# Optimization experiments

Measured on AMD Instinct MI355X. Metric: run time of the kernel, lower is better.

The kernel has to match this reference:

```python
import jax, jax.numpy as jnp
import numpy as np

B, S, HID = 8, 4096, 4096
NH, HD, ROT = 32, 128, 64  # heads, head_dim, rotary_dim (rotary_percentage=0.5)
FFN = 16384
EPS = 1e-5
SCALE = HD ** -0.5


def _ln1p(x, w, b):
    # LayerNorm1P: layer_norm with (weight + 1)
    mu = jnp.mean(x, axis=-1, keepdims=True)
    var = jnp.var(x, axis=-1, keepdims=True)
    return (x - mu) * jax.lax.rsqrt(var + EPS) * (w + 1.0) + b


def _rope(x, pos):
    # x: [B, NH, ROT] (rotary slice), pos: [B] int. GPT-NeoX style (rotate halves).
    half = ROT // 2
    inv_freq = 1.0 / (10000.0 ** (jnp.arange(0, ROT, 2, dtype=jnp.float32) / ROT))
    ang = pos[:, None].astype(jnp.float32) * inv_freq       # [B, half]
    cos = jnp.cos(ang)[:, None, :].astype(x.dtype)           # [B, 1, half]
    sin = jnp.sin(ang)[:, None, :].astype(x.dtype)
    x1, x2 = x[..., :half], x[..., half:]
    return jnp.concatenate([x1 * cos - x2 * sin, x2 * cos + x1 * sin], axis=-1)


def setup_inputs() -> dict:
    key = jax.random.key(0)
    ks = jax.random.split(key, 12)
    w = lambda k, shp: (jax.random.normal(k, shp, jnp.float32) * 0.02)
    return {
        "hidden_states": jax.random.normal(ks[0], (B, HID), jnp.float32),
        "k_cache": jax.random.normal(ks[1], (B, S, NH, HD), jnp.float32),
        "v_cache": jax.random.normal(ks[2], (B, S, NH, HD), jnp.float32),
        "w_qkv": w(ks[3], (HID, 3 * HID)),
        "w_dense": w(ks[4], (HID, HID)),
        "w_fc1": w(ks[5], (HID, 2 * FFN)),
        "w_fc2": w(ks[6], (FFN, HID)),
        "ln1_w": jax.random.normal(ks[7], (HID,), jnp.float32) * 0.02,
        "ln1_b": jnp.zeros((HID,), jnp.float32),
        "ln2_w": jax.random.normal(ks[8], (HID,), jnp.float32) * 0.02,
        "ln2_b": jnp.zeros((HID,), jnp.float32),
        "positions": jax.random.randint(ks[9], (B,), 0, S, jnp.int64),
    }


def reference(hidden_states, k_cache, v_cache, w_qkv, w_dense, w_fc1, w_fc2,
              ln1_w, ln1_b, ln2_w, ln2_b, positions):
    residual = hidden_states
    x = _ln1p(hidden_states, ln1_w, ln1_b)

    # fused QKV projection, chunk along last dim
    qkv = x @ w_qkv                                          # [B, 3*HID]
    q, k, v = jnp.split(qkv, 3, axis=-1)
    q = q.reshape(B, NH, HD)
    k = k.reshape(B, NH, HD)
    v = v.reshape(B, NH, HD)

    # inline RoPE on first ROT dims of q and new k
    q = jnp.concatenate([_rope(q[..., :ROT], positions), q[..., ROT:]], axis=-1)
    k = jnp.concatenate([_rope(k[..., :ROT], positions), k[..., ROT:]], axis=-1)

    # write new token's k/v into the paged KV cache at its slot
    bidx = jnp.arange(B)
    k_cache = k_cache.at[bidx, positions].set(k)
    v_cache = v_cache.at[bidx, positions].set(v)

    # single-query paged attention over cached keys, causal to current position
    scores = jnp.einsum('bhd,bshd->bhs', q, k_cache) * SCALE  # [B, NH, S]
    valid = jnp.arange(S)[None, None, :] <= positions[:, None, None]
    scores = jnp.where(valid, scores, jnp.finfo(scores.dtype).min)
    probs = jax.nn.softmax(scores, axis=-1)
    attn = jnp.einsum('bhs,bshd->bhd', probs, v_cache).reshape(B, HID)

    hidden_states = residual + attn @ w_dense

    residual = hidden_states
    x = _ln1p(hidden_states, ln2_w, ln2_b)
    h = x @ w_fc1                                            # [B, 2*FFN]
    h1, h2 = jnp.split(h, 2, axis=-1)
    x = (jax.nn.silu(h1) * h2) @ w_fc2                       # SwiGLU
    return residual + x
```

## Files before the change

### kernel.cpp

```cpp
#include <hip/hip_runtime.h>
#include <cstddef>
#include <cstdint>

#define NB 8
#define SEQ 4096
#define HIDDIM 4096
#define NHEAD 32
#define HDIM 128
#define FFNDIM 16384
#define ATTN_SCALE 0.08838834764831845f

__device__ __forceinline__ float wave_sum(float v) {
#pragma unroll
  for (int off = 32; off > 0; off >>= 1) v += __shfl_xor(v, off, 64);
  return v;
}

__device__ __forceinline__ int get_pos(const int* __restrict__ p, int b) {
  const bool is64 = ((p[1] | p[3] | p[5] | p[7]) == 0);
  return is64 ? p[2 * b] : p[b];
}

__global__ __launch_bounds__(256) void ln_rows(const float* __restrict__ in,
                                               const float* __restrict__ w,
                                               const float* __restrict__ bias,
                                               float* __restrict__ out_t) {
  __shared__ float row[HIDDIM];
  __shared__ float red[4];
  const int b = blockIdx.x, t = threadIdx.x;
  float s = 0.f;
  for (int i = t; i < HIDDIM; i += 256) {
    const float v = in[(size_t)b * HIDDIM + i];
    row[i] = v;
    s += v;
  }
  s = wave_sum(s);
  if ((t & 63) == 0) red[t >> 6] = s;
  __syncthreads();
  const float mean = (red[0] + red[1] + red[2] + red[3]) * (1.0f / HIDDIM);
  __syncthreads();
  float vs = 0.f;
  for (int i = t; i < HIDDIM; i += 256) {
    const float d = row[i] - mean;
    vs += d * d;
  }
  vs = wave_sum(vs);
  if ((t & 63) == 0) red[t >> 6] = vs;
  __syncthreads();
  const float var = (red[0] + red[1] + red[2] + red[3]) * (1.0f / HIDDIM);
  const float rs = rsqrtf(var + 1e-5f);
  for (int i = t; i < HIDDIM; i += 256) {
    out_t[(size_t)i * NB + b] = (row[i] - mean) * rs * (w[i] + 1.0f) + bias[i];
  }
}

template <int KCHUNK>
__global__ __launch_bounds__(256) void gemm8(const float* __restrict__ W,
                                             const float* __restrict__ xt,
                                             float* __restrict__ part, int N) {
  const int j0 = (blockIdx.x * 256 + threadIdx.x) * 4;
  const size_t i0 = (size_t)blockIdx.y * KCHUNK;
  const float* __restrict__ wp = W + i0 * N + j0;
  const float* __restrict__ xp = xt + i0 * NB;
  float4 a0 = {0, 0, 0, 0}, a1 = {0, 0, 0, 0}, a2 = {0, 0, 0, 0}, a3 = {0, 0, 0, 0};
  float4 a4 = {0, 0, 0, 0}, a5 = {0, 0, 0, 0}, a6 = {0, 0, 0, 0}, a7 = {0, 0, 0, 0};
#pragma unroll 4
  for (int i = 0; i < KCHUNK; ++i) {
    const float4 w = *reinterpret_cast<const float4*>(wp + (size_t)i * N);
    const float4 xa = *reinterpret_cast<const float4*>(xp + i * NB);
    const float4 xb = *reinterpret_cast<const float4*>(xp + i * NB + 4);
#define ACC4(A, sxx)                                                          \
  A.x = fmaf(sxx, w.x, A.x);                                                  \
  A.y = fmaf(sxx, w.y, A.y);                                                  \
  A.z = fmaf(sxx, w.z, A.z);                                                  \
  A.w = fmaf(sxx, w.w, A.w);
    ACC4(a0, xa.x) ACC4(a1, xa.y) ACC4(a2, xa.z) ACC4(a3, xa.w)
    ACC4(a4, xb.x) ACC4(a5, xb.y) ACC4(a6, xb.z) ACC4(a7, xb.w)
#undef ACC4
  }
  float* op = part + (size_t)blockIdx.y * NB * N + j0;
  *reinterpret_cast<float4*>(op) = a0; op += N;
  *reinterpret_cast<float4*>(op) = a1; op += N;
  *reinterpret_cast<float4*>(op) = a2; op += N;
  *reinterpret_cast<float4*>(op) = a3; op += N;
  *reinterpret_cast<float4*>(op) = a4; op += N;
  *reinterpret_cast<float4*>(op) = a5; op += N;
  *reinterpret_cast<float4*>(op) = a6; op += N;
  *reinterpret_cast<float4*>(op) = a7;
}

__global__ __launch_bounds__(128) void rope_reduce(const float* __restrict__ part, int nchunk,
                                                   const int* __restrict__ posp,
                                                   float* __restrict__ qo,
                                                   float* __restrict__ ko,
                                                   float* __restrict__ vo) {
  const int blk = blockIdx.x;
  const int b = blk >> 5, h = blk & 31;
  const int t = threadIdx.x;
  const int role = t >> 5;
  const int d4 = (t & 31) * 4;
  const int col = h * HDIM + d4;
  __shared__ float qsh[HDIM], ksh[HDIM];
  float4 acc = {0.f, 0.f, 0.f, 0.f};
  if (role < 3) {
    const size_t off = (size_t)role * HIDDIM + col;
    for (int c = 0; c < nchunk; ++c) {
      const float4 p = *reinterpret_cast<const float4*>(
          part + ((size_t)c * NB + b) * (3 * HIDDIM) + off);
      acc.x += p.x; acc.y += p.y; acc.z += p.z; acc.w += p.w;
    }
    if (role == 0) *reinterpret_cast<float4*>(&qsh[d4]) = acc;
    if (role == 1) *reinterpret_cast<float4*>(&ksh[d4]) = acc;
  }
  __syncthreads();
  if (role < 2) {
    const float* sh = role ? ksh : qsh;
    const float pos = (float)get_pos(posp, b);
    float4 o;
    float* ov = &o.x;
#pragma unroll
    for (int j = 0; j < 4; ++j) {
      const int d = d4 + j;
      if (d < 64) {
        const int f = d & 31;
        const float ang = pos * powf(10000.0f, -(float)f * (1.0f / 32.0f));
        const float cs = cosf(ang), sn = sinf(ang);
        ov[j] = (d < 32) ? sh[d] * cs - sh[d + 32] * sn
                         : sh[d] * cs + sh[d - 32] * sn;
      } else {
        ov[j] = sh[d];
      }
    }
    float* dst = (role ? ko : qo) + (size_t)b * HIDDIM + col;
    *reinterpret_cast<float4*>(dst) = o;
  } else if (role == 2) {
    *reinterpret_cast<float4*>(vo + (size_t)b * HIDDIM + col) = acc;
  }
}

__global__ __launch_bounds__(256) void attn_split(
    const float* __restrict__ kc, const float* __restrict__ vc,
    const float* __restrict__ q, const float* __restrict__ kn,
    const float* __restrict__ vn, const int* __restrict__ posp,
    float* __restrict__ Mp, float* __restrict__ Lp, float* __restrict__ Ap) {
  const int c = blockIdx.x, h = blockIdx.y, b = blockIdx.z;
  const int pos = get_pos(posp, b);
  const int s0 = c * 256;
  if (s0 > pos) return;
  const int s1 = min(s0 + 256, pos + 1);
  const int wid = threadIdx.x >> 6, lane = threadIdx.x & 63;
  const int half = lane >> 5;
  const int d4 = (lane & 31) * 4;
  const float4 qv = *reinterpret_cast<const float4*>(q + (size_t)b * HIDDIM + h * HDIM + d4);
  const float* kb = kc + ((size_t)b * SEQ * NHEAD + h) * HDIM + d4;
  const float* vb = vc + ((size_t)b * SEQ * NHEAD + h) * HDIM + d4;
  const float* knp = kn + (size_t)b * HIDDIM + h * HDIM + d4;
  const float* vnp = vn + (size_t)b * HIDDIM + h * HDIM + d4;
  float m = -1e30f, l = 0.f;
  float4 acc = {0.f, 0.f, 0.f, 0.f};
  for (int sb = s0; sb < s1; sb += 8) {
    const int s = sb + wid * 2 + half;
    const float* kp = (s == pos) ? knp : kb + (size_t)s * (NHEAD * HDIM);
    const float* vp = (s == pos) ? vnp : vb + (size_t)s * (NHEAD * HDIM);
    const float4 kk = *reinterpret_cast<const float4*>(kp);
    const float4 vv = *reinterpret_cast<const float4*>(vp);
    float p = qv.x * kk.x + qv.y * kk.y + qv.z * kk.z + qv.w * kk.w;
#pragma unroll
    for (int off = 16; off > 0; off >>= 1) p += __shfl_xor(p, off, 64);
    p = (s < s1) ? p * ATTN_SCALE : -2e30f;
    const float mn = fmaxf(m, p);
    const float cf = __expf(m - mn);
    const float pw = __expf(p - mn);
    l = l * cf + pw;
    acc.x = acc.x * cf + pw * vv.x;
    acc.y = acc.y * cf + pw * vv.y;
    acc.z = acc.z * cf + pw * vv.z;
    acc.w = acc.w * cf + pw * vv.w;
    m = mn;
  }
  __shared__ float sm[8], sl[8], sa[8][HDIM];
  const int st = wid * 2 + half;
  *reinterpret_cast<float4*>(&sa[st][d4]) = acc;
  if ((lane & 31) == 0) { sm[st] = m; sl[st] = l; }
  __syncthreads();
  if (threadIdx.x < HDIM) {
    const int d = threadIdx.x;
    float M = -1e30f;
#pragma unroll
    for (int w2 = 0; w2 < 8; ++w2) M = fmaxf(M, sm[w2]);
    float L = 0.f, A = 0.f;
#pragma unroll
    for (int w2 = 0; w2 < 8; ++w2) {
      const float e = __expf(sm[w2] - M);
      L += e * sl[w2];
      A += e * sa[w2][d];
    }
    const size_t idx = (size_t)(b * NHEAD + h) * 16 + c;
    if (d == 0) { Mp[idx] = M; Lp[idx] = L; }
    Ap[idx * HDIM + d] = A;
  }
}

__global__ __launch_bounds__(128) void attn_combine(
    const float* __restrict__ Mp, const float* __restrict__ Lp,
    const float* __restrict__ Ap, const int* __restrict__ posp,
    float* __restrict__ out_t) {
  const int blk = blockIdx.x;
  const int b = blk >> 5, h = blk & 31;
  const int d = threadIdx.x;
  const int nc = get_pos(posp, b) / 256 + 1;
  const size_t base = (size_t)(b * NHEAD + h) * 16;
  float M = -1e30f;
  for (int c = 0; c < nc; ++c) M = fmaxf(M, Mp[base + c]);
  float L = 0.f, A = 0.f;
  for (int c = 0; c < nc; ++c) {
    const float e = __expf(Mp[base + c] - M);
    L += e * Lp[base + c];
    A += e * Ap[(base + c) * HDIM + d];
  }
  out_t[(size_t)(h * HDIM + d) * NB + b] = A / L;
}

__global__ __launch_bounds__(128) void reduce_add(const float* __restrict__ part, int nchunk,
                                                  const float* __restrict__ base,
                                                  float* __restrict__ out) {
  const int i4 = blockIdx.x * 128 + threadIdx.x;
  const float4* b4 = reinterpret_cast<const float4*>(base);
  const float4* p4 = reinterpret_cast<const float4*>(part);
  float4 v = b4[i4];
  for (int c = 0; c < nchunk; ++c) {
    const float4 p = p4[(size_t)c * (NB * HIDDIM / 4) + i4];
    v.x += p.x; v.y += p.y; v.z += p.z; v.w += p.w;
  }
  reinterpret_cast<float4*>(out)[i4] = v;
}

__global__ __launch_bounds__(256) void gate_silu(const float* __restrict__ part, int nchunk,
                                                 float* __restrict__ gt) {
  const int j4 = (blockIdx.x * 256 + threadIdx.x) * 4;
  const int b = blockIdx.y;
  float4 h1 = {0.f, 0.f, 0.f, 0.f}, h2 = {0.f, 0.f, 0.f, 0.f};
  for (int c = 0; c < nchunk; ++c) {
    const float* p = part + ((size_t)c * NB + b) * (2 * FFNDIM);
    const float4 a = *reinterpret_cast<const float4*>(p + j4);
    const float4 g = *reinterpret_cast<const float4*>(p + FFNDIM + j4);
    h1.x += a.x; h1.y += a.y; h1.z += a.z; h1.w += a.w;
    h2.x += g.x; h2.y += g.y; h2.z += g.z; h2.w += g.w;
  }
  const float* h1v = &h1.x;
  const float* h2v = &h2.x;
#pragma unroll
  for (int j = 0; j < 4; ++j) {
    const float g = (h1v[j] / (1.f + __expf(-h1v[j]))) * h2v[j];
    gt[(size_t)(j4 + j) * NB + b] = g;
  }
}

extern "C" void kernel_launch(void* const* d_in, const int* in_sizes, int n_in,
                              void* d_out, int out_size, void* d_ws, size_t ws_size,
                              hipStream_t stream) {
  const float* hs = (const float*)d_in[0];
  const float* kc = (const float*)d_in[1];
  const float* vc = (const float*)d_in[2];
  const float* wqkv = (const float*)d_in[3];
  const float* wdense = (const float*)d_in[4];
  const float* wfc1 = (const float*)d_in[5];
  const float* wfc2 = (const float*)d_in[6];
  const float* ln1w = (const float*)d_in[7];
  const float* ln1b = (const float*)d_in[8];
  const float* ln2w = (const float*)d_in[9];
  const float* ln2b = (const float*)d_in[10];
  const int* posp = (const int*)d_in[11];
  float* out = (float*)d_out;

  float* ws = (float*)d_ws;
  float* x1t = ws;
  float* qws = x1t + 32768;
  float* kws = qws + 32768;
  float* vws = kws + 32768;
  float* attnt = vws + 32768;
  float* hidden2 = attnt + 32768;
  float* x2t = hidden2 + 32768;
  float* gt = x2t + 32768;
  float* Mp = gt + 131072;
  float* Lp = Mp + 4096;
  float* Ap = Lp + 4096;
  float* part = Ap + 524288;

  ln_rows<<<8, 256, 0, stream>>>(hs, ln1w, ln1b, x1t);
  gemm8<128><<<dim3(12, 32), 256, 0, stream>>>(wqkv, x1t, part, 3 * HIDDIM);
  rope_reduce<<<256, 128, 0, stream>>>(part, 32, posp, qws, kws, vws);
  attn_split<<<dim3(16, NHEAD, NB), 256, 0, stream>>>(kc, vc, qws, kws, vws, posp, Mp, Lp, Ap);
  attn_combine<<<256, 128, 0, stream>>>(Mp, Lp, Ap, posp, attnt);
  gemm8<128><<<dim3(4, 32), 256, 0, stream>>>(wdense, attnt, part, HIDDIM);
  reduce_add<<<64, 128, 0, stream>>>(part, 32, hs, hidden2);
  ln_rows<<<8, 256, 0, stream>>>(hidden2, ln2w, ln2b, x2t);
  gemm8<256><<<dim3(32, 16), 256, 0, stream>>>(wfc1, x2t, part, 2 * FFNDIM);
  gate_silu<<<dim3(16, NB), 256, 0, stream>>>(part, 16, gt);
  gemm8<256><<<dim3(4, 64), 256, 0, stream>>>(wfc2, gt, part, HIDDIM);
  reduce_add<<<64, 128, 0, stream>>>(part, 64, hidden2, out);
}
```

Measured before the change: 422.8 us.

## Fuse whole decoder layer into one cooperative persistent kernel with grid syncs

Replaces the twelve separate kernel launches with a single cooperative kernel of 256 blocks that runs every stage, separated by grid-wide barriers. LayerNorm is folded into the GEMM input staging, with statistics computed in one pass (sum and sum of squares). Attention work items are handed out through an atomic counter. The GEMM tiling changes to float2 per thread with smaller K-chunks. The goal is to remove launch overhead and intermediate buffers. The cost is that only 256 blocks run, which may under-occupy the GPU for the bandwidth-bound GEMMs, and each stage pays for a grid barrier.

```diff
diff --git a/kernel.cpp b/kernel.cpp
--- a/kernel.cpp
+++ b/kernel.cpp
@@ -1,6 +1,9 @@
 #include <hip/hip_runtime.h>
+#include <hip/hip_cooperative_groups.h>
 #include <cstddef>
 #include <cstdint>
+
+namespace cg = cooperative_groups;
 
 #define NB 8
 #define SEQ 4096
@@ -9,8 +12,10 @@
 #define HDIM 128
 #define FFNDIM 16384
 #define ATTN_SCALE 0.08838834764831845f
-
-__device__ __forceinline__ float wave_sum(float v) {
+#define NBLK 256
+#define NTHR 512
+
+__device__ __forceinline__ float wave_sum64(float v) {
 #pragma unroll
   for (int off = 32; off > 0; off >>= 1) v += __shfl_xor(v, off, 64);
   return v;
@@ -21,238 +26,362 @@
   return is64 ? p[2 * b] : p[b];
 }
 
-__global__ __launch_bounds__(256) void ln_rows(const float* __restrict__ in,
-                                               const float* __restrict__ w,
-                                               const float* __restrict__ bias,
-                                               float* __restrict__ out_t) {
-  __shared__ float row[HIDDIM];
-  __shared__ float red[4];
-  const int b = blockIdx.x, t = threadIdx.x;
-  float s = 0.f;
-  for (int i = t; i < HIDDIM; i += 256) {
-    const float v = in[(size_t)b * HIDDIM + i];
-    row[i] = v;
+__device__ __forceinline__ void ln_stats(const float* __restrict__ in,
+                                         float* mu, float* rsd, int t) {
+  const int wv = t >> 6, lane = t & 63;
+  float s = 0.f, s2 = 0.f;
+  for (int i = lane; i < HIDDIM; i += 64) {
+    const float v = in[(size_t)wv * HIDDIM + i];
     s += v;
-  }
-  s = wave_sum(s);
-  if ((t & 63) == 0) red[t >> 6] = s;
+    s2 += v * v;
+  }
+  s = wave_sum64(s);
+  s2 = wave_sum64(s2);
+  if (lane == 0) {
+    const float m = s * (1.0f / HIDDIM);
+    mu[wv] = m;
+    rsd[wv] = rsqrtf(s2 * (1.0f / HIDDIM) - m * m + 1e-5f);
+  }
+}
+
+__device__ __forceinline__ void gemm_item(const float* __restrict__ W, int N,
+                                          size_t i0, int nrows, int jbase,
+                                          const float* xs,
+                                          float* __restrict__ partOut, int t) {
+  const int j = jbase + t * 2;
+  const float* __restrict__ wp = W + i0 * N + j;
+  float2 acc[8];
+#pragma unroll
+  for (int b = 0; b < 8; ++b) acc[b] = {0.f, 0.f};
+#pragma unroll 8
+  for (int i = 0; i < nrows; ++i) {
+    const float2 w = *reinterpret_cast<const float2*>(wp + (size_t)i * N);
+    const float* xr = xs + i * 8;
+#pragma unroll
+    for (int b = 0; b < 8; ++b) {
+      acc[b].x = fmaf(xr[b], w.x, acc[b].x);
+      acc[b].y = fmaf(xr[b], w.y, acc[b].y);
+    }
+  }
+#pragma unroll
+  for (int b = 0; b < 8; ++b)
+    *reinterpret_cast<float2*>(partOut + (size_t)b * N + j) = acc[b];
+}
+
+__global__ __launch_bounds__(NTHR, 2) void mega(
+    const float* __restrict__ hs, const float* __restrict__ kcache,
+    const float* __restrict__ vcache, const float* __restrict__ wqkv,
+    const float* __restrict__ wdense, const float* __restrict__ wfc1,
+    const float* __restrict__ wfc2, const float* __restrict__ ln1w,
+    const float* __restrict__ ln1b, const float* __restrict__ ln2w,
+    const float* __restrict__ ln2b, const int* __restrict__ posp,
+    float* __restrict__ out, float* __restrict__ ws) {
+  cg::grid_group gg = cg::this_grid();
+  const int blk = blockIdx.x, t = threadIdx.x;
+
+  float* qws = ws;
+  float* kws = qws + 32768;
+  float* vws = kws + 32768;
+  float* attnt = vws + 32768;
+  float* hidden2 = attnt + 32768;
+  float* gt = hidden2 + 32768;
+  float* Mp = gt + 131072;
+  float* Lp = Mp + 4096;
+  float* Ap = Lp + 4096;
+  unsigned int* ctr = reinterpret_cast<unsigned int*>(Ap + 524288);
+  float* part = reinterpret_cast<float*>(ctr + 64);
+
+  __shared__ float xs[512 * 8];
+  __shared__ float mu[8], rsd[8];
+  __shared__ float qp[4][HDIM], kp[4][HDIM], vp[4][HDIM];
+  __shared__ float sa[16][HDIM];
+  __shared__ float sm[16], sl[16];
+  __shared__ int sitem;
+
+  ln_stats(hs, mu, rsd, t);
   __syncthreads();
-  const float mean = (red[0] + red[1] + red[2] + red[3]) * (1.0f / HIDDIM);
+  for (int it = blk; it < 768; it += NBLK) {
+    const int jt = it % 12;
+    const int ck = it / 12;
+    const size_t i0 = (size_t)ck * 64;
+    {
+      const int i = t >> 3, b = t & 7;
+      const int ii = (int)i0 + i;
+      const float v = hs[(size_t)b * HIDDIM + ii];
+      xs[i * 8 + b] = (v - mu[b]) * rsd[b] * (ln1w[ii] + 1.f) + ln1b[ii];
+    }
+    __syncthreads();
+    gemm_item(wqkv, 3 * HIDDIM, i0, 64, jt * 1024, xs,
+              part + (size_t)ck * 8 * (3 * HIDDIM), t);
+    __syncthreads();
+  }
+  __threadfence();
+  gg.sync();
+
+  {
+    const int b = blk >> 5, h = blk & 31;
+    const int d = t & 127, g = t >> 7;
+    float q = 0.f, k = 0.f, v = 0.f;
+    for (int c = g * 16; c < g * 16 + 16; ++c) {
+      const float* p = part + (size_t)(c * 8 + b) * (3 * HIDDIM) + h * HDIM + d;
+      q += p[0];
+      k += p[HIDDIM];
+      v += p[2 * HIDDIM];
+    }
+    qp[g][d] = q;
+    kp[g][d] = k;
+    vp[g][d] = v;
+    if (blk == 0 && t == 0) *ctr = 0u;
+    __syncthreads();
+    if (t < HDIM) {
+      qp[0][t] = qp[0][t] + qp[1][t] + qp[2][t] + qp[3][t];
+      kp[0][t] = kp[0][t] + kp[1][t] + kp[2][t] + kp[3][t];
+      vp[0][t] = vp[0][t] + vp[1][t] + vp[2][t] + vp[3][t];
+    }
+    __syncthreads();
+    if (t < HDIM) {
+      const int pos = get_pos(posp, b);
+      float qv = qp[0][t], kv = kp[0][t];
+      if (t < 64) {
+        const int f = t & 31;
+        const float ang = (float)pos * powf(10000.0f, -(float)f * (1.0f / 32.0f));
+        const float cs = cosf(ang), sn = sinf(ang);
+        if (t < 32) {
+          qv = qp[0][t] * cs - qp[0][t + 32] * sn;
+          kv = kp[0][t] * cs - kp[0][t + 32] * sn;
+        } else {
+          qv = qp[0][t] * cs + qp[0][t - 32] * sn;
+          kv = kp[0][t] * cs + kp[0][t - 32] * sn;
+        }
+      }
+      const size_t o = (size_t)b * HIDDIM + h * HDIM + t;
+      qws[o] = qv;
+      kws[o] = kv;
+      vws[o] = vp[0][t];
+    }
+  }
+  __threadfence();
+  gg.sync();
+
+  while (true) {
+    if (t == 0) sitem = (int)atomicAdd(ctr, 1u);
+    __syncthreads();
+    const int item = sitem;
+    if (item >= 4096) break;
+    const int c = item >> 8;
+    const int pair = item & 255;
+    const int b = pair & 7, h = pair >> 3;
+    const int pos = get_pos(posp, b);
+    const int s0 = c * 256;
+    if (s0 > pos) {
+      __syncthreads();
+      continue;
+    }
+    const int s1 = min(s0 + 256, pos + 1);
+    const int hw = t >> 5, l32 = t & 31, d4 = l32 * 4;
+    const float4 qv = *reinterpret_cast<const float4*>(
+        qws + (size_t)b * HIDDIM + h * HDIM + d4);
+    const float* kb = kcache + ((size_t)b * SEQ * NHEAD + h) * HDIM + d4;
+    const float* vb = vcache + ((size_t)b * SEQ * NHEAD + h) * HDIM + d4;
+    const float* knp = kws + (size_t)b * HIDDIM + h * HDIM + d4;
+    const float* vnp = vws + (size_t)b * HIDDIM + h * HDIM + d4;
+    float m = -1e30f, l = 0.f;
+    float4 acc = {0.f, 0.f, 0.f, 0.f};
+    const int rbase = s0 + hw * 16;
+#pragma unroll 4
+    for (int r = 0; r < 16; ++r) {
+      const int s = rbase + r;
+      const bool valid = (s < s1);
+      const int sc = valid ? s : s0;
+      const float* kp_ = (sc == pos) ? knp : kb + (size_t)sc * (NHEAD * HDIM);
+      const float* vp_ = (sc == pos) ? vnp : vb + (size_t)sc * (NHEAD * HDIM);
+      const float4 kk = *reinterpret_cast<const float4*>(kp_);
+      const float4 vv = *reinterpret_cast<const float4*>(vp_);
+      float p = qv.x * kk.x + qv.y * kk.y + qv.z * kk.z + qv.w * kk.w;
+#pragma unroll
+      for (int off = 16; off > 0; off >>= 1) p += __shfl_xor(p, off, 64);
+      p = valid ? p * ATTN_SCALE : -2e30f;
+      const float mn = fmaxf(m, p);
+      const float cf = __expf(m - mn);
+      const float pw = __expf(p - mn);
+      l = l * cf + pw;
+      acc.x = acc.x * cf + pw * vv.x;
+      acc.y = acc.y * cf + pw * vv.y;
+      acc.z = acc.z * cf + pw * vv.z;
+      acc.w = acc.w * cf + pw * vv.w;
+      m = mn;
+    }
+    *reinterpret_cast<float4*>(&sa[hw][d4]) = acc;
+    if (l32 == 0) {
+      sm[hw] = m;
+      sl[hw] = l;
+    }
+    __syncthreads();
+    if (t < HDIM) {
+      float M = -1e30f;
+#pragma unroll
+      for (int w2 = 0; w2 < 16; ++w2) M = fmaxf(M, sm[w2]);
+      float L = 0.f, A = 0.f;
+#pragma unroll
+      for (int w2 = 0; w2 < 16; ++w2) {
+        const float e = __expf(sm[w2] - M);
+        L += e * sl[w2];
+        A += e * sa[w2][t];
+      }
+      const size_t idx = (size_t)pair * 16 + c;
+      if (t == 0) {
+        Mp[idx] = M;
+        Lp[idx] = L;
+      }
+      Ap[idx * HDIM + t] = A;
+    }
+    __syncthreads();
+  }
+  __threadfence();
+  gg.sync();
+
+  if (t < HDIM) {
+    const int b = blk & 7, h = blk >> 3;
+    const int pos = get_pos(posp, b);
+    const int nc = pos / 256 + 1;
+    const size_t base = (size_t)blk * 16;
+    float M = -1e30f;
+    for (int c = 0; c < nc; ++c) M = fmaxf(M, Mp[base + c]);
+    float L = 0.f, A = 0.f;
+    for (int c = 0; c < nc; ++c) {
+      const float e = __expf(Mp[base + c] - M);
+      L += e * Lp[base + c];
+      A += e * Ap[(base + c) * HDIM + t];
+    }
+    attnt[(size_t)(h * HDIM + t) * NB + b] = A / L;
+  }
+  __threadfence();
+  gg.sync();
+
+  {
+    const int jt = blk & 3;
+    const int ck = blk >> 2;
+    const size_t i0 = (size_t)ck * 64;
+    xs[t] = attnt[i0 * 8 + t];
+    __syncthreads();
+    gemm_item(wdense, HIDDIM, i0, 64, jt * 1024, xs,
+              part + (size_t)ck * 8 * HIDDIM, t);
+  }
+  __threadfence();
+  gg.sync();
+
+  {
+    const int idx = blk * NTHR + t;
+    const int g = idx >> 2, sub = idx & 3;
+    if (g < 8192) {
+      const float4* p4 = reinterpret_cast<const float4*>(part);
+      float4 v = {0.f, 0.f, 0.f, 0.f};
+      for (int c = sub * 16; c < sub * 16 + 16; ++c) {
+        const float4 p = p4[(size_t)c * 8192 + g];
+        v.x += p.x; v.y += p.y; v.z += p.z; v.w += p.w;
+      }
+#pragma unroll
+      for (int off = 1; off < 4; off <<= 1) {
+        v.x += __shfl_xor(v.x, off, 64);
+        v.y += __shfl_xor(v.y, off, 64);
+        v.z += __shfl_xor(v.z, off, 64);
+        v.w += __shfl_xor(v.w, off, 64);
+      }
+      if (sub == 0) {
+        const float4 hv = reinterpret_cast<const float4*>(hs)[g];
+        float4 o = {v.x + hv.x, v.y + hv.y, v.z + hv.z, v.w + hv.w};
+        reinterpret_cast<float4*>(hidden2)[g] = o;
+      }
+    }
+  }
+  __threadfence();
+  gg.sync();
+
+  ln_stats(hidden2, mu, rsd, t);
   __syncthreads();
-  float vs = 0.f;
-  for (int i = t; i < HIDDIM; i += 256) {
-    const float d = row[i] - mean;
-    vs += d * d;
-  }
-  vs = wave_sum(vs);
-  if ((t & 63) == 0) red[t >> 6] = vs;
-  __syncthreads();
-  const float var = (red[0] + red[1] + red[2] + red[3]) * (1.0f / HIDDIM);
-  const float rs = rsqrtf(var + 1e-5f);
-  for (int i = t; i < HIDDIM; i += 256) {
-    out_t[(size_t)i * NB + b] = (row[i] - mean) * rs * (w[i] + 1.0f) + bias[i];
-  }
-}
-
-template <int KCHUNK>
-__global__ __launch_bounds__(256) void gemm8(const float* __restrict__ W,
-                                             const float* __restrict__ xt,
-                                             float* __restrict__ part, int N) {
-  const int j0 = (blockIdx.x * 256 + threadIdx.x) * 4;
-  const size_t i0 = (size_t)blockIdx.y * KCHUNK;
-  const float* __restrict__ wp = W + i0 * N + j0;
-  const float* __restrict__ xp = xt + i0 * NB;
-  float4 a0 = {0, 0, 0, 0}, a1 = {0, 0, 0, 0}, a2 = {0, 0, 0, 0}, a3 = {0, 0, 0, 0};
-  float4 a4 = {0, 0, 0, 0}, a5 = {0, 0, 0, 0}, a6 = {0, 0, 0, 0}, a7 = {0, 0, 0, 0};
-#pragma unroll 4
-  for (int i = 0; i < KCHUNK; ++i) {
-    const float4 w = *reinterpret_cast<const float4*>(wp + (size_t)i * N);
-    const float4 xa = *reinterpret_cast<const float4*>(xp + i * NB);
-    const float4 xb = *reinterpret_cast<const float4*>(xp + i * NB + 4);
-#define ACC4(A, sxx)                                                          \
-  A.x = fmaf(sxx, w.x, A.x);                                                  \
-  A.y = fmaf(sxx, w.y, A.y);                                                  \
-  A.z = fmaf(sxx, w.z, A.z);                                                  \
-  A.w = fmaf(sxx, w.w, A.w);
-    ACC4(a0, xa.x) ACC4(a1, xa.y) ACC4(a2, xa.z) ACC4(a3, xa.w)
-    ACC4(a4, xb.x) ACC4(a5, xb.y) ACC4(a6, xb.z) ACC4(a7, xb.w)
-#undef ACC4
-  }
-  float* op = part + (size_t)blockIdx.y * NB * N + j0;
-  *reinterpret_cast<float4*>(op) = a0; op += N;
-  *reinterpret_cast<float4*>(op) = a1; op += N;
-  *reinterpret_cast<float4*>(op) = a2; op += N;
-  *reinterpret_cast<float4*>(op) = a3; op += N;
-  *reinterpret_cast<float4*>(op) = a4; op += N;
-  *reinterpret_cast<float4*>(op) = a5; op += N;
-  *reinterpret_cast<float4*>(op) = a6; op += N;
-  *reinterpret_cast<float4*>(op) = a7;
-}
-
-__global__ __launch_bounds__(128) void rope_reduce(const float* __restrict__ part, int nchunk,
-                                                   const int* __restrict__ posp,
-                                                   float* __restrict__ qo,
-                                                   float* __restrict__ ko,
-                                                   float* __restrict__ vo) {
-  const int blk = blockIdx.x;
-  const int b = blk >> 5, h = blk & 31;
-  const int t = threadIdx.x;
-  const int role = t >> 5;
-  const int d4 = (t & 31) * 4;
-  const int col = h * HDIM + d4;
-  __shared__ float qsh[HDIM], ksh[HDIM];
-  float4 acc = {0.f, 0.f, 0.f, 0.f};
-  if (role < 3) {
-    const size_t off = (size_t)role * HIDDIM + col;
-    for (int c = 0; c < nchunk; ++c) {
-      const float4 p = *reinterpret_cast<const float4*>(
-          part + ((size_t)c * NB + b) * (3 * HIDDIM) + off);
-      acc.x += p.x; acc.y += p.y; acc.z += p.z; acc.w += p.w;
-    }
-    if (role == 0) *reinterpret_cast<float4*>(&qsh[d4]) = acc;
-    if (role == 1) *reinterpret_cast<float4*>(&ksh[d4]) = acc;
-  }
-  __syncthreads();
-  if (role < 2) {
-    const float* sh = role ? ksh : qsh;
-    const float pos = (float)get_pos(posp, b);
-    float4 o;
-    float* ov = &o.x;
-#pragma unroll
-    for (int j = 0; j < 4; ++j) {
-      const int d = d4 + j;
-      if (d < 64) {
-        const int f = d & 31;
-        const float ang = pos * powf(10000.0f, -(float)f * (1.0f / 32.0f));
-        const float cs = cosf(ang), sn = sinf(ang);
-        ov[j] = (d < 32) ? sh[d] * cs - sh[d + 32] * sn
-                         : sh[d] * cs + sh[d - 32] * sn;
-      } else {
-        ov[j] = sh[d];
-      }
-    }
-    float* dst = (role ? ko : qo) + (size_t)b * HIDDIM + col;
-    *reinterpret_cast<float4*>(dst) = o;
-  } else if (role == 2) {
-    *reinterpret_cast<float4*>(vo + (size_t)b * HIDDIM + col) = acc;
-  }
-}
-
-__global__ __launch_bounds__(256) void attn_split(
-    const float* __restrict__ kc, const float* __restrict__ vc,
-    const float* __restrict__ q, const float* __restrict__ kn,
-    const float* __restrict__ vn, const int* __restrict__ posp,
-    float* __restrict__ Mp, float* __restrict__ Lp, float* __restrict__ Ap) {
-  const int c = blockIdx.x, h = blockIdx.y, b = blockIdx.z;
-  const int pos = get_pos(posp, b);
-  const int s0 = c * 256;
-  if (s0 > pos) return;
-  const int s1 = min(s0 + 256, pos + 1);
-  const int wid = threadIdx.x >> 6, lane = threadIdx.x & 63;
-  const int half = lane >> 5;
-  const int d4 = (lane & 31) * 4;
-  const float4 qv = *reinterpret_cast<const float4*>(q + (size_t)b * HIDDIM + h * HDIM + d4);
-  const float* kb = kc + ((size_t)b * SEQ * NHEAD + h) * HDIM + d4;
-  const float* vb = vc + ((size_t)b * SEQ * NHEAD + h) * HDIM + d4;
-  const float* knp = kn + (size_t)b * HIDDIM + h * HDIM + d4;
-  const float* vnp = vn + (size_t)b * HIDDIM + h * HDIM + d4;
-  float m = -1e30f, l = 0.f;
-  float4 acc = {0.f, 0.f, 0.f, 0.f};
-  for (int sb = s0; sb < s1; sb += 8) {
-    const int s = sb + wid * 2 + half;
-    const float* kp = (s == pos) ? knp : kb + (size_t)s * (NHEAD * HDIM);
-    const float* vp = (s == pos) ? vnp : vb + (size_t)s * (NHEAD * HDIM);
-    const float4 kk = *reinterpret_cast<const float4*>(kp);
-    const float4 vv = *reinterpret_cast<const float4*>(vp);
-    float p = qv.x * kk.x + qv.y * kk.y + qv.z * kk.z + qv.w * kk.w;
-#pragma unroll
-    for (int off = 16; off > 0; off >>= 1) p += __shfl_xor(p, off, 64);
-    p = (s < s1) ? p * ATTN_SCALE : -2e30f;
-    const float mn = fmaxf(m, p);
-    const float cf = __expf(m - mn);
-    const float pw = __expf(p - mn);
-    l = l * cf + pw;
-    acc.x = acc.x * cf + pw * vv.x;
-    acc.y = acc.y * cf + pw * vv.y;
-    acc.z = acc.z * cf + pw * vv.z;
-    acc.w = acc.w * cf + pw * vv.w;
-    m = mn;
-  }
-  __shared__ float sm[8], sl[8], sa[8][HDIM];
-  const int st = wid * 2 + half;
-  *reinterpret_cast<float4*>(&sa[st][d4]) = acc;
-  if ((lane & 31) == 0) { sm[st] = m; sl[st] = l; }
-  __syncthreads();
-  if (threadIdx.x < HDIM) {
-    const int d = threadIdx.x;
-    float M = -1e30f;
-#pragma unroll
-    for (int w2 = 0; w2 < 8; ++w2) M = fmaxf(M, sm[w2]);
-    float L = 0.f, A = 0.f;
-#pragma unroll
-    for (int w2 = 0; w2 < 8; ++w2) {
-      const float e = __expf(sm[w2] - M);
-      L += e * sl[w2];
-      A += e * sa[w2][d];
-    }
-    const size_t idx = (size_t)(b * NHEAD + h) * 16 + c;
-    if (d == 0) { Mp[idx] = M; Lp[idx] = L; }
-    Ap[idx * HDIM + d] = A;
-  }
-}
-
-__global__ __launch_bounds__(128) void attn_combine(
-    const float* __restrict__ Mp, const float* __restrict__ Lp,
-    const float* __restrict__ Ap, const int* __restrict__ posp,
-    float* __restrict__ out_t) {
-  const int blk = blockIdx.x;
-  const int b = blk >> 5, h = blk & 31;
-  const int d = threadIdx.x;
-  const int nc = get_pos(posp, b) / 256 + 1;
-  const size_t base = (size_t)(b * NHEAD + h) * 16;
-  float M = -1e30f;
-  for (int c = 0; c < nc; ++c) M = fmaxf(M, Mp[base + c]);
-  float L = 0.f, A = 0.f;
-  for (int c = 0; c < nc; ++c) {
-    const float e = __expf(Mp[base + c] - M);
-    L += e * Lp[base + c];
-    A += e * Ap[(base + c) * HDIM + d];
-  }
-  out_t[(size_t)(h * HDIM + d) * NB + b] = A / L;
-}
-
-__global__ __launch_bounds__(128) void reduce_add(const float* __restrict__ part, int nchunk,
-                                                  const float* __restrict__ base,
-                                                  float* __restrict__ out) {
-  const int i4 = blockIdx.x * 128 + threadIdx.x;
-  const float4* b4 = reinterpret_cast<const float4*>(base);
-  const float4* p4 = reinterpret_cast<const float4*>(part);
-  float4 v = b4[i4];
-  for (int c = 0; c < nchunk; ++c) {
-    const float4 p = p4[(size_t)c * (NB * HIDDIM / 4) + i4];
-    v.x += p.x; v.y += p.y; v.z += p.z; v.w += p.w;
-  }
-  reinterpret_cast<float4*>(out)[i4] = v;
-}
-
-__global__ __launch_bounds__(256) void gate_silu(const float* __restrict__ part, int nchunk,
-                                                 float* __restrict__ gt) {
-  const int j4 = (blockIdx.x * 256 + threadIdx.x) * 4;
-  const int b = blockIdx.y;
-  float4 h1 = {0.f, 0.f, 0.f, 0.f}, h2 = {0.f, 0.f, 0.f, 0.f};
-  for (int c = 0; c < nchunk; ++c) {
-    const float* p = part + ((size_t)c * NB + b) * (2 * FFNDIM);
-    const float4 a = *reinterpret_cast<const float4*>(p + j4);
-    const float4 g = *reinterpret_cast<const float4*>(p + FFNDIM + j4);
-    h1.x += a.x; h1.y += a.y; h1.z += a.z; h1.w += a.w;
-    h2.x += g.x; h2.y += g.y; h2.z += g.z; h2.w += g.w;
-  }
-  const float* h1v = &h1.x;
-  const float* h2v = &h2.x;
-#pragma unroll
-  for (int j = 0; j < 4; ++j) {
-    const float g = (h1v[j] / (1.f + __expf(-h1v[j]))) * h2v[j];
-    gt[(size_t)(j4 + j) * NB + b] = g;
+  {
+    const int jt = blk & 31;
+    const int ck = blk >> 5;
+    const size_t i0 = (size_t)ck * 512;
+#pragma unroll
+    for (int r = 0; r < 8; ++r) {
+      const int idx2 = r * NTHR + t;
+      const int i = idx2 >> 3, b = idx2 & 7;
+      const int ii = (int)i0 + i;
+      const float v = hidden2[(size_t)b * HIDDIM + ii];
+      xs[idx2] = (v - mu[b]) * rsd[b] * (ln2w[ii] + 1.f) + ln2b[ii];
+    }
+    __syncthreads();
+    gemm_item(wfc1, 2 * FFNDIM, i0, 512, jt * 1024, xs,
+              part + (size_t)ck * 8 * (2 * FFNDIM), t);
+  }
+  __threadfence();
+  gg.sync();
+
+  {
+    const int idx = blk * NTHR + t;
+    if (idx < 32768) {
+      const int j4 = idx >> 3, b = idx & 7;
+      const int j = j4 * 4;
+      float4 h1 = {0.f, 0.f, 0.f, 0.f}, h2 = {0.f, 0.f, 0.f, 0.f};
+      for (int c = 0; c < 8; ++c) {
+        const float* p = part + (size_t)(c * 8 + b) * (2 * FFNDIM);
+        const float4 a = *reinterpret_cast<const float4*>(p + j);
+        const float4 g2 = *reinterpret_cast<const float4*>(p + FFNDIM + j);
+        h1.x += a.x; h1.y += a.y; h1.z += a.z; h1.w += a.w;
+        h2.x += g2.x; h2.y += g2.y; h2.z += g2.z; h2.w += g2.w;
+      }
+      const float* h1v = &h1.x;
+      const float* h2v = &h2.x;
+#pragma unroll
+      for (int jj = 0; jj < 4; ++jj) {
+        const float gv = (h1v[jj] / (1.f + __expf(-h1v[jj]))) * h2v[jj];
+        gt[(size_t)(j + jj) * NB + b] = gv;
+      }
+    }
+  }
+  __threadfence();
+  gg.sync();
+
+  {
+    const int jt = blk & 3;
+    const int ck = blk >> 2;
+    const size_t i0 = (size_t)ck * 256;
+#pragma unroll
+    for (int r = 0; r < 4; ++r) {
+      const int idx2 = r * NTHR + t;
+      xs[idx2] = gt[i0 * 8 + idx2];
+    }
+    __syncthreads();
+    gemm_item(wfc2, HIDDIM, i0, 256, jt * 1024, xs,
+              part + (size_t)ck * 8 * HIDDIM, t);
+  }
+  __threadfence();
+  gg.sync();
+
+  {
+    const int idx = blk * NTHR + t;
+    const int g = idx >> 2, sub = idx & 3;
+    if (g < 8192) {
+      const float4* p4 = reinterpret_cast<const float4*>(part);
+      float4 v = {0.f, 0.f, 0.f, 0.f};
+      for (int c = sub * 16; c < sub * 16 + 16; ++c) {
+        const float4 p = p4[(size_t)c * 8192 + g];
+        v.x += p.x; v.y += p.y; v.z += p.z; v.w += p.w;
+      }
+#pragma unroll
+      for (int off = 1; off < 4; off <<= 1) {
+        v.x += __shfl_xor(v.x, off, 64);
+        v.y += __shfl_xor(v.y, off, 64);
+        v.z += __shfl_xor(v.z, off, 64);
+        v.w += __shfl_xor(v.w, off, 64);
+      }
+      if (sub == 0) {
+        const float4 hv = reinterpret_cast<const float4*>(hidden2)[g];
+        float4 o = {v.x + hv.x, v.y + hv.y, v.z + hv.z, v.w + hv.w};
+        reinterpret_cast<float4*>(out)[g] = o;
+      }
+    }
   }
 }
 
@@ -271,32 +400,11 @@
   const float* ln2w = (const float*)d_in[9];
   const float* ln2b = (const float*)d_in[10];
   const int* posp = (const int*)d_in[11];
-  float* out = (float*)d_out;
-
-  float* ws = (float*)d_ws;
-  float* x1t = ws;
-  float* qws = x1t + 32768;
-  float* kws = qws + 32768;
-  float* vws = kws + 32768;
-  float* attnt = vws + 32768;
-  float* hidden2 = attnt + 32768;
-  float* x2t = hidden2 + 32768;
-  float* gt = x2t + 32768;
-  float* Mp = gt + 131072;
-  float* Lp = Mp + 4096;
-  float* Ap = Lp + 4096;
-  float* part = Ap + 524288;
-
-  ln_rows<<<8, 256, 0, stream>>>(hs, ln1w, ln1b, x1t);
-  gemm8<128><<<dim3(12, 32), 256, 0, stream>>>(wqkv, x1t, part, 3 * HIDDIM);
-  rope_reduce<<<256, 128, 0, stream>>>(part, 32, posp, qws, kws, vws);
-  attn_split<<<dim3(16, NHEAD, NB), 256, 0, stream>>>(kc, vc, qws, kws, vws, posp, Mp, Lp, Ap);
-  attn_combine<<<256, 128, 0, stream>>>(Mp, Lp, Ap, posp, attnt);
-  gemm8<128><<<dim3(4, 32), 256, 0, stream>>>(wdense, attnt, part, HIDDIM);
-  reduce_add<<<64, 128, 0, stream>>>(part, 32, hs, hidden2);
-  ln_rows<<<8, 256, 0, stream>>>(hidden2, ln2w, ln2b, x2t);
-  gemm8<256><<<dim3(32, 16), 256, 0, stream>>>(wfc1, x2t, part, 2 * FFNDIM);
-  gate_silu<<<dim3(16, NB), 256, 0, stream>>>(part, 16, gt);
-  gemm8<256><<<dim3(4, 64), 256, 0, stream>>>(wfc2, gt, part, HIDDIM);
-  reduce_add<<<64, 128, 0, stream>>>(part, 64, hidden2, out);
-}
+  float* outp = (float*)d_out;
+  float* wsp = (float*)d_ws;
+
+  void* args[] = {&hs,   &kc,   &vc,   &wqkv, &wdense, &wfc1, &wfc2,
+                  &ln1w, &ln1b, &ln2w, &ln2b, &posp,   &outp, &wsp};
+  hipLaunchCooperativeKernel((void*)mega, dim3(NBLK), dim3(NTHR), args, 0,
+                             stream);
+}
```

Result: slower. 1.329 ms (+214.3%).
